# Kernel optimization log

Measured on AMD Instinct MI355X. Metric: run time of the kernel, lower is better.

The kernel has to match this reference:

```python
import jax, jax.numpy as jnp
import numpy as np

# Dims: batch, seq, model dim, heads, routes-per-query, bleed-over alpha
B, S, D, H, K_ROUTES = 4, 512, 1024, 16, 64
HD = D // H                      # head_dim = 64
SCALE = 1.0 / float(np.sqrt(HD))
ALPHA = 0.25                     # neighbor bleed-over (forward arg default 0.0; >0 here)
CAUSAL = True
NEG = jnp.float32(-1e9)


def _build_routes(seq_len: int, k: int, depth: int = 8) -> np.ndarray:
    """Cantor-coordinate based positional routes (mirrors _build_positional_routes)."""
    pos = np.arange(seq_len, dtype=np.float64)
    x = pos / max(1, seq_len - 1)
    x = np.clip(x, 1e-6, 1.0 - 1e-6)
    val = np.zeros_like(x)
    factor = 0.5
    for _ in range(depth):
        xs = x * 3.0
        digit = xs.astype(np.int64)
        frac = xs - digit
        val = val + (digit == 2).astype(np.float64) * factor
        x = frac
        factor *= 0.5
    coords = np.clip(val, 0.0, 1.0)
    dist = np.abs(coords[:, None] - coords[None, :])            # [S,S]
    routes = np.argsort(dist, axis=1, kind='stable')[:, :k]     # k smallest distances
    return routes.astype(np.int32)


def setup_inputs() -> dict:
    key = jax.random.key(0)
    k0, k1, k2 = jax.random.split(key, 3)
    x = jax.random.normal(k0, (B, S, D), dtype=jnp.float32)
    # nn.Linear weights stored pre-transposed as [in, out] for clean matmul
    w_qkv = jax.random.normal(k1, (D, 3 * D), dtype=jnp.float32) * (1.0 / np.sqrt(D))
    b_qkv = jnp.zeros((3 * D,), dtype=jnp.float32)
    w_out = jax.random.normal(k2, (D, D), dtype=jnp.float32) * (1.0 / np.sqrt(D))
    b_out = jnp.zeros((D,), dtype=jnp.float32)
    routes = jnp.asarray(_build_routes(S, K_ROUTES), dtype=jnp.int32)  # [S, K]
    return {"x": x, "w_qkv": w_qkv, "b_qkv": b_qkv,
            "w_out": w_out, "b_out": b_out, "routes": routes}


def reference(x, w_qkv, b_qkv, w_out, b_out, routes):
    # QKV projection: [B,S,3D] -> [3,B,H,S,hd]
    qkv = (x @ w_qkv + b_qkv).reshape(B, S, 3, H, HD).transpose(2, 0, 3, 1, 4)
    q, k, v = qkv[0], qkv[1], qkv[2]                 # each [B,H,S,hd]

    r = routes                                        # [S,K]
    k_g = jnp.take(k, r, axis=2)                      # [B,H,S,K,hd]
    v_g = jnp.take(v, r, axis=2)
    if ALPHA > 0.0:
        rl = jnp.clip(r - 1, 0, S - 1)
        rr = jnp.clip(r + 1, 0, S - 1)
        k_g = (1.0 - ALPHA) * k_g + (ALPHA / 2.0) * (jnp.take(k, rl, axis=2) + jnp.take(k, rr, axis=2))
        v_g = (1.0 - ALPHA) * v_g + (ALPHA / 2.0) * (jnp.take(v, rl, axis=2) + jnp.take(v, rr, axis=2))

    scores = jnp.einsum('bhqd,bhqkd->bhqk', q, k_g) * SCALE   # [B,H,S,K]
    if CAUSAL:
        # route index > query position is masked (each query always routes to itself)
        mask = r > jnp.arange(S, dtype=r.dtype)[:, None]       # [S,K]
        scores = jnp.where(mask[None, None], NEG, scores)

    attn = jax.nn.softmax(scores, axis=-1)
    out = jnp.einsum('bhqk,bhqkd->bhqd', attn, v_g)            # [B,H,S,hd]
    out = out.transpose(0, 2, 1, 3).reshape(B, S, D)
    return out @ w_out + b_out
```

## Files before the change

### kernel.cpp

```cpp
#include <hip/hip_runtime.h>
#include <hip/hip_bf16.h>

#define BB 4
#define SS 512
#define DD 1024
#define HH 16
#define KR 64
#define HDIM 64
#define THREE_D 3072
#define M_ROWS 2048
#define SCALE_F 0.125f
#define SCALE_LOG2E 0.1803368801111144f

typedef __attribute__((ext_vector_type(8))) short short8;
typedef __attribute__((ext_vector_type(4))) float floatx4;

union F8 { short8 s; unsigned int u[4]; unsigned short h[8]; };

__device__ inline float bfu(unsigned short h){ union{unsigned int u; float f;} c; c.u = ((unsigned int)h) << 16; return c.f; }
__device__ inline unsigned short f2bf(float f){
    union{float f; unsigned int u;} c; c.f = f;
    unsigned int u = c.u;
    return (unsigned short)((u + 0x7fffu + ((u >> 16) & 1u)) >> 16);
}

#define GLOAD_LDS16(g, l)                                                     \
    __builtin_amdgcn_global_load_lds(                                         \
        (const __attribute__((address_space(1))) unsigned int*)(g),           \
        (__attribute__((address_space(3))) unsigned int*)(l), 16, 0, 0)

__global__ __launch_bounds__(256) void prep_kernel(
    const float* __restrict__ x, const float* __restrict__ w_qkv,
    const float* __restrict__ w_out, const int* __restrict__ routes,
    unsigned short* __restrict__ xb_sw, unsigned short* __restrict__ wb1_sw,
    unsigned short* __restrict__ wb2_sw, unsigned int* __restrict__ maskg)
{
    const int bx = blockIdx.x;
    const int tid = threadIdx.x;
    if (bx < 1024) {
        int gid = bx * 256 + tid;
        int r  = gid & 127;
        int c  = (gid >> 7) & 3;
        int kt = (gid >> 9) & 31;
        int mt = gid >> 14;
        const float* src = x + ((size_t)(mt * 128 + r)) * 1024 + kt * 32 + c * 8;
        float4 a = *(const float4*)src;
        float4 b = *(const float4*)(src + 4);
        F8 o;
        o.h[0] = f2bf(a.x); o.h[1] = f2bf(a.y); o.h[2] = f2bf(a.z); o.h[3] = f2bf(a.w);
        o.h[4] = f2bf(b.x); o.h[5] = f2bf(b.y); o.h[6] = f2bf(b.z); o.h[7] = f2bf(b.w);
        *(uint4*)(xb_sw + (size_t)gid * 8) = *(uint4*)&o;
    } else if (bx < 3072) {
        const float* w;
        unsigned short* out;
        int gid, N;
        if (bx < 2560) { w = w_qkv; out = wb1_sw; N = THREE_D; gid = (bx - 1024) * 256 + tid; }
        else           { w = w_out; out = wb2_sw; N = DD;      gid = (bx - 2560) * 256 + tid; }
        int r  = gid & 127;
        int c  = (gid >> 7) & 3;
        int kt = (gid >> 9) & 31;
        int nt = gid >> 14;
        int n = nt * 128 + r;
        int kbase = kt * 32 + c * 8;
        F8 o;
#pragma unroll
        for (int j = 0; j < 8; ++j)
            o.h[j] = f2bf(w[(size_t)(kbase + j) * N + n]);
        *(uint4*)(out + (size_t)gid * 8) = *(uint4*)&o;
    } else {
        int q = (bx - 3072) * 256 + tid;
        unsigned int w[16];
#pragma unroll
        for (int i = 0; i < 16; ++i) w[i] = 0u;
        for (int j = 0; j < KR; ++j) {
            int r = routes[q * KR + j];
            if (r <= q) w[r >> 5] |= 1u << (r & 31);
        }
#pragma unroll
        for (int sw = 0; sw < 16; ++sw) maskg[sw * SS + q] = w[sw];
    }
}

__global__ __launch_bounds__(256) void gemm_qkv(
    const unsigned short* __restrict__ Asw,
    const unsigned short* __restrict__ Bsw,
    const float* __restrict__ bias,
    unsigned short* __restrict__ qb, unsigned short* __restrict__ kb,
    unsigned short* __restrict__ vb)
{
    __shared__ __align__(16) unsigned short Sh[24576];
    unsigned short* Alds = Sh;
    unsigned short* Blds = Sh + 8192;

    const int tid  = threadIdx.x;
    const int lane = tid & 63;
    const int wid  = tid >> 6;
    const int l15  = lane & 15;
    const int quad = lane >> 4;

    const int bid  = blockIdx.x;
    const int xcd  = bid & 7;
    const int loc  = bid >> 3;
    const int mt64 = (xcd & 3) * 8 + (loc & 7);
    const int nt   = (xcd >> 2) * 12 + (loc >> 3);

    const int mt = mt64 >> 1;
    const int rh = (mt64 & 1) * 64;
    const int wn = wid * 32;

    floatx4 acc[4][2];
#pragma unroll
    for (int i = 0; i < 4; ++i)
#pragma unroll
        for (int j = 0; j < 2; ++j) acc[i][j] = (floatx4){0.f, 0.f, 0.f, 0.f};

    for (int kt8 = 0; kt8 < 8; ++kt8) {
#pragma unroll
        for (int kh = 0; kh < 4; ++kh) {
            int kt = kt8 * 4 + kh;
            const unsigned short* ga = Asw + ((size_t)(mt * 32 + kt) * 4 + wid) * 1024 + (rh + lane) * 8;
            const unsigned short* gb = Bsw + (size_t)(nt * 32 + kt) * 4096 + wid * 1024 + lane * 8;
            GLOAD_LDS16(ga,       Alds + kh * 2048 + wid * 512 + lane * 8);
            GLOAD_LDS16(gb,       Blds + kh * 4096 + wid * 1024 + lane * 8);
            GLOAD_LDS16(gb + 512, Blds + kh * 4096 + wid * 1024 + 512 + lane * 8);
        }
        __syncthreads();

#pragma unroll
        for (int kh = 0; kh < 4; ++kh) {
            F8 af[4], bf[2];
#pragma unroll
            for (int mi = 0; mi < 4; ++mi)
                af[mi] = *(const F8*)(Alds + kh * 2048 + (size_t)(quad * 64 + mi * 16 + l15) * 8);
#pragma unroll
            for (int ni = 0; ni < 2; ++ni)
                bf[ni] = *(const F8*)(Blds + kh * 4096 + (size_t)(quad * 128 + wn + ni * 16 + l15) * 8);
#pragma unroll
            for (int mi = 0; mi < 4; ++mi)
#pragma unroll
                for (int ni = 0; ni < 2; ++ni)
                    acc[mi][ni] = __builtin_amdgcn_mfma_f32_16x16x32_bf16(
                        af[mi].s, bf[ni].s, acc[mi][ni], 0, 0, 0);
        }
        __syncthreads();
    }

    const int m0 = mt64 * 64;
    const int n0 = nt * 128;

#pragma unroll
    for (int mi = 0; mi < 4; ++mi) {
#pragma unroll
        for (int ni = 0; ni < 2; ++ni) {
            int col = wn + ni * 16 + l15;
            float bv = bias[n0 + col];
#pragma unroll
            for (int r = 0; r < 4; ++r) {
                int row = mi * 16 + quad * 4 + r;
                Sh[row * 136 + col] = f2bf(acc[mi][ni][r] + bv);
            }
        }
    }
    __syncthreads();

    for (int i = tid; i < 1024; i += 256) {
        int rr = i >> 4, cc = i & 15;
        int grow = m0 + rr, gcol = n0 + cc * 8;
        int b = grow >> 9, s = grow & 511;
        int which = gcol >> 10, rem = gcol & 1023;
        int h = rem >> 6, hd = rem & 63;
        unsigned short* dst = (which == 0) ? qb : (which == 1) ? kb : vb;
        uint4 val = *(const uint4*)(Sh + rr * 136 + cc * 8);
        *(uint4*)(dst + (((size_t)(b * HH + h) * SS) + s) * HDIM + hd) = val;
    }
}

__global__ __launch_bounds__(256) void gemm_out(
    const unsigned short* __restrict__ Asw,
    const unsigned short* __restrict__ Bsw,
    const float* __restrict__ bias,
    float* __restrict__ Cout)
{
    __shared__ __align__(16) unsigned short Alds[8192];
    __shared__ __align__(16) unsigned short Blds[8192];

    const int tid  = threadIdx.x;
    const int lane = tid & 63;
    const int wid  = tid >> 6;
    const int l15  = lane & 15;
    const int quad = lane >> 4;

    const int bid  = blockIdx.x;
    const int xcd  = bid & 7;
    const int loc  = bid >> 3;
    const int mt64 = (xcd & 3) * 8 + (loc & 7);
    const int nt64 = (xcd >> 2) * 8 + (loc >> 3);

    const int mt  = mt64 >> 1;
    const int rh  = (mt64 & 1) * 64;
    const int ntB = nt64 >> 1;
    const int rhB = (nt64 & 1) * 64;
    const int wm  = (wid >> 1) * 32;
    const int wn  = (wid & 1) * 32;

    floatx4 acc[2][2];
#pragma unroll
    for (int i = 0; i < 2; ++i)
#pragma unroll
        for (int j = 0; j < 2; ++j) acc[i][j] = (floatx4){0.f, 0.f, 0.f, 0.f};

    for (int kt4 = 0; kt4 < 8; ++kt4) {
#pragma unroll
        for (int kh = 0; kh < 4; ++kh) {
            int kt = kt4 * 4 + kh;
            const unsigned short* ga = Asw + ((size_t)(mt  * 32 + kt) * 4 + wid) * 1024 + (rh  + lane) * 8;
            const unsigned short* gb = Bsw + ((size_t)(ntB * 32 + kt) * 4 + wid) * 1024 + (rhB + lane) * 8;
            GLOAD_LDS16(ga, Alds + kh * 2048 + wid * 512 + lane * 8);
            GLOAD_LDS16(gb, Blds + kh * 2048 + wid * 512 + lane * 8);
        }
        __syncthreads();

#pragma unroll
        for (int kh = 0; kh < 4; ++kh) {
            F8 af[2], bf[2];
#pragma unroll
            for (int mi = 0; mi < 2; ++mi)
                af[mi] = *(const F8*)(Alds + kh * 2048 + (size_t)(quad * 64 + wm + mi * 16 + l15) * 8);
#pragma unroll
            for (int ni = 0; ni < 2; ++ni)
                bf[ni] = *(const F8*)(Blds + kh * 2048 + (size_t)(quad * 64 + wn + ni * 16 + l15) * 8);
#pragma unroll
            for (int mi = 0; mi < 2; ++mi)
#pragma unroll
                for (int ni = 0; ni < 2; ++ni)
                    acc[mi][ni] = __builtin_amdgcn_mfma_f32_16x16x32_bf16(
                        af[mi].s, bf[ni].s, acc[mi][ni], 0, 0, 0);
        }
        __syncthreads();
    }

    const int m0 = mt64 * 64;
    const int n0 = nt64 * 64;
#pragma unroll
    for (int mi = 0; mi < 2; ++mi) {
#pragma unroll
        for (int ni = 0; ni < 2; ++ni) {
            int col = n0 + wn + ni * 16 + l15;
            float bv = bias[col];
#pragma unroll
            for (int r = 0; r < 4; ++r) {
                int row = m0 + wm + mi * 16 + quad * 4 + r;
                Cout[(size_t)row * DD + col] = acc[mi][ni][r] + bv;
            }
        }
    }
}

__global__ __launch_bounds__(256) void blend_kv_kernel(
    const unsigned short* __restrict__ kb, const unsigned short* __restrict__ vb,
    unsigned short* __restrict__ K2g, unsigned short* __restrict__ Vtg)
{
    __shared__ float vt[130][65];
    const int bh = blockIdx.x >> 2;
    const int qd = blockIdx.x & 3;
    const int s0 = qd * 128;
    const int tid = threadIdx.x;
    const unsigned short* kbase = kb + (size_t)bh * SS * HDIM;
    const unsigned short* vbase = vb + (size_t)bh * SS * HDIM;
    unsigned short* Kq = K2g + ((size_t)(bh * 4 + qd)) * 8192;
    unsigned short* Vq = Vtg + ((size_t)(bh * 4 + qd)) * 8192;

    for (int i = tid; i < 130 * 8; i += 256) {
        int row = i >> 3, c8 = (i & 7) << 3;
        int s = s0 + row - 1; s = s < 0 ? 0 : (s > SS - 1 ? SS - 1 : s);
        F8 vv = *(const F8*)(vbase + (size_t)s * 64 + c8);
#pragma unroll
        for (int j = 0; j < 8; ++j) vt[row][c8 + j] = bfu(vv.h[j]);
    }

    for (int i = tid; i < 1024; i += 256) {
        int sl = i >> 3, cc = i & 7;
        int s = s0 + sl;
        int sm = s ? s - 1 : 0;
        int sp = (s < SS - 1) ? s + 1 : SS - 1;
        F8 k0 = *(const F8*)(kbase + (size_t)s  * 64 + cc * 8);
        F8 km = *(const F8*)(kbase + (size_t)sm * 64 + cc * 8);
        F8 kp = *(const F8*)(kbase + (size_t)sp * 64 + cc * 8);
        F8 o;
#pragma unroll
        for (int j = 0; j < 8; ++j)
            o.h[j] = f2bf(0.75f * bfu(k0.h[j]) + 0.125f * (bfu(km.h[j]) + bfu(kp.h[j])));
        *(uint4*)(Kq + (size_t)(sl * 8 + (cc ^ (sl & 7))) * 8) = *(uint4*)&o;
    }
    __syncthreads();

    for (int i = tid; i < 1024; i += 256) {
        int d = i >> 4, scl = i & 15;
        F8 o;
#pragma unroll
        for (int a = 0; a < 8; ++a) {
            int rl = scl * 8 + a;
            o.h[a] = f2bf(0.75f * vt[rl + 1][d] + 0.125f * (vt[rl][d] + vt[rl + 2][d]));
        }
        int chunk = d * 16 + (scl & 8) + ((scl ^ d) & 7);
        *(uint4*)(Vq + (size_t)chunk * 8) = *(uint4*)&o;
    }
}

__global__ __launch_bounds__(256) void attn_kernel(
    const unsigned short* __restrict__ qb,
    const unsigned short* __restrict__ K2g,
    const unsigned short* __restrict__ Vtg,
    const unsigned int* __restrict__ maskg,
    unsigned short* __restrict__ attn_sw)
{
    __shared__ __align__(16) unsigned short Ks2[2][8192];
    __shared__ __align__(16) unsigned short Vs2[2][8192];
    __shared__ __align__(16) unsigned short Ps[4096];

    const int bid = blockIdx.x;
    const int xcd = bid & 7;
    const int loc = bid >> 3;
    const int bh  = xcd * 8 + (loc & 7);
    const int qt8 = loc >> 3;
    const int qt  = (qt8 < 4) ? qt8 : 11 - qt8;
    const int b = bh >> 4, h = bh & 15;
    const int tid  = threadIdx.x;
    const int lane = tid & 63;
    const int wid  = tid >> 6;
    const int l15  = lane & 15;
    const int quad = lane >> 4;

    const int nq    = (qt >> 1) + 1;
    const int qmaxw = qt * 64 + wid * 16 + 15;

    const unsigned short* Kbh = K2g + (size_t)bh * 4 * 8192;
    const unsigned short* Vbh = Vtg + (size_t)bh * 4 * 8192;

    #define STAGE(qd, bufi) do {                                              \
        const unsigned short* kq = Kbh + (size_t)(qd) * 8192 + wid * 2048;    \
        const unsigned short* vq = Vbh + (size_t)(qd) * 8192 + wid * 2048;    \
        unsigned short* kl = Ks2[bufi] + wid * 2048;                          \
        unsigned short* vl = Vs2[bufi] + wid * 2048;                          \
        GLOAD_LDS16(kq + lane * 8,        kl + lane * 8);                     \
        GLOAD_LDS16(kq + 512 + lane * 8,  kl + 512 + lane * 8);               \
        GLOAD_LDS16(kq + 1024 + lane * 8, kl + 1024 + lane * 8);              \
        GLOAD_LDS16(kq + 1536 + lane * 8, kl + 1536 + lane * 8);              \
        GLOAD_LDS16(vq + lane * 8,        vl + lane * 8);                     \
        GLOAD_LDS16(vq + 512 + lane * 8,  vl + 512 + lane * 8);               \
        GLOAD_LDS16(vq + 1024 + lane * 8, vl + 1024 + lane * 8);              \
        GLOAD_LDS16(vq + 1536 + lane * 8, vl + 1536 + lane * 8);              \
    } while (0)

    const int q = qt * 64 + wid * 16 + l15;

    F8 qf[2];
    {
        const unsigned short* qrow = qb + ((size_t)bh * SS + q) * 64;
        qf[0] = *(const F8*)(qrow + quad * 8);
        qf[1] = *(const F8*)(qrow + 32 + quad * 8);
    }

    STAGE(0, 0);
    __syncthreads();

    floatx4 accO[4];
#pragma unroll
    for (int dt = 0; dt < 4; ++dt) accO[dt] = (floatx4){0.f, 0.f, 0.f, 0.f};
    float lsum = 0.f;
    unsigned int* Pw = (unsigned int*)Ps + wid * 512;

    for (int qd = 0; qd < nq; ++qd) {
        if (qd + 1 < nq) STAGE(qd + 1, (qd + 1) & 1);
        const unsigned short* Ksb = Ks2[qd & 1];
        const unsigned short* Vsb = Vs2[qd & 1];
        const int sbase128 = qd * 128;

        floatx4 accS[8];
#pragma unroll
        for (int st = 0; st < 8; ++st) {
            if (sbase128 + (st >> 2) * 64 <= qmaxw) {
                int srow = st * 16 + l15;
                const F8 k0 = *(const F8*)(Ksb + (((srow << 3) | ( quad      ^ (srow & 7))) << 3));
                const F8 k1 = *(const F8*)(Ksb + (((srow << 3) | ((4 + quad) ^ (srow & 7))) << 3));
                floatx4 a = (floatx4){0.f, 0.f, 0.f, 0.f};
                a = __builtin_amdgcn_mfma_f32_16x16x32_bf16(k0.s, qf[0].s, a, 0, 0, 0);
                a = __builtin_amdgcn_mfma_f32_16x16x32_bf16(k1.s, qf[1].s, a, 0, 0, 0);
                accS[st] = a;
            }
        }

#pragma unroll
        for (int ch2 = 0; ch2 < 2; ++ch2) {
            if (sbase128 + ch2 * 64 > qmaxw) continue;
            unsigned int mw0 = maskg[(qd * 4 + ch2 * 2) * SS + q];
            unsigned int mw1 = maskg[(qd * 4 + ch2 * 2 + 1) * SS + q];
#pragma unroll
            for (int t = 0; t < 4; ++t) {
                unsigned int mw = (t & 2) ? mw1 : mw0;
                int sbase = (t & 1) * 16 + quad * 4;
                floatx4 a = accS[ch2 * 4 + t];
                float e0 = ((mw >> (sbase + 0)) & 1u) ? exp2f(a[0] * SCALE_LOG2E) : 0.f;
                float e1 = ((mw >> (sbase + 1)) & 1u) ? exp2f(a[1] * SCALE_LOG2E) : 0.f;
                float e2 = ((mw >> (sbase + 2)) & 1u) ? exp2f(a[2] * SCALE_LOG2E) : 0.f;
                float e3 = ((mw >> (sbase + 3)) & 1u) ? exp2f(a[3] * SCALE_LOG2E) : 0.f;
                lsum += (e0 + e1) + (e2 + e3);
                unsigned int w0 = (unsigned int)f2bf(e0) | ((unsigned int)f2bf(e1) << 16);
                unsigned int w1 = (unsigned int)f2bf(e2) | ((unsigned int)f2bf(e3) << 16);
                int off0 = t * 8 + quad * 2;
                int off1 = off0 + 1;
                Pw[l15 * 32 + ((((off0 >> 2) ^ (l15 & 7)) << 2) | (off0 & 3))] = w0;
                Pw[l15 * 32 + ((((off1 >> 2) ^ (l15 & 7)) << 2) | (off1 & 3))] = w1;
            }
            F8 pa[2];
#pragma unroll
            for (int ks = 0; ks < 2; ++ks) {
                int ci = ks * 4 + quad;
                pa[ks] = *(const F8*)((const unsigned short*)(Pw + l15 * 32) +
                                      ((ci ^ (l15 & 7)) << 3));
            }
#pragma unroll
            for (int dt = 0; dt < 4; ++dt) {
                int d = dt * 16 + l15;
#pragma unroll
                for (int ks = 0; ks < 2; ++ks) {
                    int scl = ch2 * 8 + ks * 4 + quad;
                    int chunk = d * 16 + (scl & 8) + ((scl ^ d) & 7);
                    const F8 bv = *(const F8*)(Vsb + ((size_t)chunk << 3));
                    accO[dt] = __builtin_amdgcn_mfma_f32_16x16x32_bf16(pa[ks].s, bv.s, accO[dt], 0, 0, 0);
                }
            }
        }
        __syncthreads();
    }

    lsum += __shfl_xor(lsum, 16);
    lsum += __shfl_xor(lsum, 32);
    float inv = 1.0f / lsum;

    unsigned short* Ow = Ps + wid * 1024;
#pragma unroll
    for (int r = 0; r < 4; ++r) {
        float invr = __shfl(inv, quad * 4 + r);
#pragma unroll
        for (int dt = 0; dt < 4; ++dt)
            Ow[(quad * 4 + r) * 64 + dt * 16 + l15] = f2bf(accO[dt][r] * invr);
    }
#pragma unroll
    for (int i = 0; i < 2; ++i) {
        int ch = i * 64 + lane;
        int qlocal = ch >> 3, j = ch & 7;
        int qq = qt * 64 + wid * 16 + qlocal;
        int mrow = b * SS + qq;
        int mt = mrow >> 7, rr = mrow & 127;
        int kt2 = h * 2 + (j >> 2), c = j & 3;
        size_t gid = (((size_t)(mt * 32 + kt2) * 4 + c) * 128 + rr);
        *(uint4*)(attn_sw + gid * 8) = *(const uint4*)(Ow + qlocal * 64 + j * 8);
    }
    #undef STAGE
}

extern "C" void kernel_launch(void* const* d_in, const int* in_sizes, int n_in,
                              void* d_out, int out_size, void* d_ws, size_t ws_size,
                              hipStream_t stream)
{
    const float* x     = (const float*)d_in[0];
    const float* w_qkv = (const float*)d_in[1];
    const float* b_qkv = (const float*)d_in[2];
    const float* w_out = (const float*)d_in[3];
    const float* b_out = (const float*)d_in[4];
    const int* routes  = (const int*)d_in[5];

    char* w = (char*)d_ws;
    unsigned short* xb_sw  = (unsigned short*)(w);
    unsigned short* wb1_sw = (unsigned short*)(w + (4u  << 20));
    unsigned short* wb2_sw = (unsigned short*)(w + (10u << 20));
    unsigned short* qbuf   = (unsigned short*)(w + (12u << 20));
    unsigned short* kbuf   = (unsigned short*)(w + (16u << 20));
    unsigned short* vbuf   = (unsigned short*)(w + (20u << 20));
    unsigned short* K2g    = (unsigned short*)(w + (24u << 20));
    unsigned short* Vtg    = (unsigned short*)(w + (28u << 20));
    unsigned short* attnsw = (unsigned short*)(w + (32u << 20));
    unsigned int*   maskg  = (unsigned int*)(w + (36u << 20));

    prep_kernel<<<3074, 256, 0, stream>>>(x, w_qkv, w_out, routes,
                                          xb_sw, wb1_sw, wb2_sw, maskg);

    gemm_qkv<<<768, 256, 0, stream>>>(xb_sw, wb1_sw, b_qkv, qbuf, kbuf, vbuf);

    blend_kv_kernel<<<256, 256, 0, stream>>>(kbuf, vbuf, K2g, Vtg);

    attn_kernel<<<512, 256, 0, stream>>>(qbuf, K2g, Vtg, maskg, attnsw);

    gemm_out<<<512, 256, 0, stream>>>(attnsw, wb2_sw, b_out, (float*)d_out);
}
```

Measured before the change: 141.4 us.

## Fuse neighbor K/V blending into QKV GEMM epilogue, drop blend kernel

The QKV GEMM now computes an extra 16-row halo for K/V tiles so the neighbor bleed-over blend can be done in registers via lane shuffles in the epilogue. It writes the blended K and transposed V directly in the swizzled layouts the attention kernel expects. This removes the separate blend kernel launch and the round trip of raw K/V through global memory. In exchange, K/V blocks do about 25% more MFMA work and load extra A rows, and the epilogue is more complex, with boundary handling at sequence edges.

```diff
diff --git a/kernel.cpp b/kernel.cpp
--- a/kernel.cpp
+++ b/kernel.cpp
@@ -81,16 +81,16 @@
     }
 }
 
-__global__ __launch_bounds__(256) void gemm_qkv(
+__global__ __launch_bounds__(256, 3) void gemm_qkv_fused(
     const unsigned short* __restrict__ Asw,
     const unsigned short* __restrict__ Bsw,
     const float* __restrict__ bias,
-    unsigned short* __restrict__ qb, unsigned short* __restrict__ kb,
-    unsigned short* __restrict__ vb)
+    unsigned short* __restrict__ qb,
+    unsigned short* __restrict__ K2g,
+    unsigned short* __restrict__ Vtg)
 {
-    __shared__ __align__(16) unsigned short Sh[24576];
-    unsigned short* Alds = Sh;
-    unsigned short* Blds = Sh + 8192;
+    __shared__ __align__(16) unsigned short Sh[26624];
+    unsigned short* Blds = Sh + 10240;
 
     const int tid  = threadIdx.x;
     const int lane = tid & 63;
@@ -104,13 +104,21 @@
     const int mt64 = (xcd & 3) * 8 + (loc & 7);
     const int nt   = (xcd >> 2) * 12 + (loc >> 3);
 
-    const int mt = mt64 >> 1;
-    const int rh = (mt64 & 1) * 64;
-    const int wn = wid * 32;
-
-    floatx4 acc[4][2];
-#pragma unroll
-    for (int i = 0; i < 4; ++i)
+    const bool isQ = (nt < 8);
+    const int m0   = mt64 * 64;
+    const int n0   = nt * 128;
+    const int wn   = wid * 32;
+    const int base_m = isQ ? m0 : (m0 - 8);
+
+    int rA = base_m + lane;        rA = rA < 0 ? 0 : (rA > 2047 ? 2047 : rA);
+    int rB = base_m + 64 + l15;    rB = rB < 0 ? 0 : (rB > 2047 ? 2047 : rB);
+    const int cB = lane >> 4;
+    const size_t aOffA = ((size_t)(rA >> 7) * 128) * 1024 + (size_t)(rA & 127) * 8;
+    const size_t aOffB = ((size_t)(rB >> 7) * 128) * 1024 + (size_t)(rB & 127) * 8;
+
+    floatx4 acc[5][2];
+#pragma unroll
+    for (int i = 0; i < 5; ++i)
 #pragma unroll
         for (int j = 0; j < 2; ++j) acc[i][j] = (floatx4){0.f, 0.f, 0.f, 0.f};
 
@@ -118,9 +126,13 @@
 #pragma unroll
         for (int kh = 0; kh < 4; ++kh) {
             int kt = kt8 * 4 + kh;
-            const unsigned short* ga = Asw + ((size_t)(mt * 32 + kt) * 4 + wid) * 1024 + (rh + lane) * 8;
+            const unsigned short* ga = Asw + aOffA + (size_t)(kt * 4 + wid) * 1024;
+            GLOAD_LDS16(ga, Sh + kh * 2560 + wid * 512 + lane * 8);
+            if (!isQ && wid == 0) {
+                const unsigned short* ga2 = Asw + aOffB + (size_t)(kt * 4 + cB) * 1024;
+                GLOAD_LDS16(ga2, Sh + kh * 2560 + 2048 + lane * 8);
+            }
             const unsigned short* gb = Bsw + (size_t)(nt * 32 + kt) * 4096 + wid * 1024 + lane * 8;
-            GLOAD_LDS16(ga,       Alds + kh * 2048 + wid * 512 + lane * 8);
             GLOAD_LDS16(gb,       Blds + kh * 4096 + wid * 1024 + lane * 8);
             GLOAD_LDS16(gb + 512, Blds + kh * 4096 + wid * 1024 + 512 + lane * 8);
         }
@@ -128,50 +140,107 @@
 
 #pragma unroll
         for (int kh = 0; kh < 4; ++kh) {
-            F8 af[4], bf[2];
-#pragma unroll
-            for (int mi = 0; mi < 4; ++mi)
-                af[mi] = *(const F8*)(Alds + kh * 2048 + (size_t)(quad * 64 + mi * 16 + l15) * 8);
+            F8 af[5], bf[2];
+#pragma unroll
+            for (int emi = 0; emi < 4; ++emi)
+                af[emi] = *(const F8*)(Sh + kh * 2560 + (size_t)(quad * 64 + emi * 16 + l15) * 8);
+            if (!isQ)
+                af[4] = *(const F8*)(Sh + kh * 2560 + 2048 + (size_t)(quad * 16 + l15) * 8);
 #pragma unroll
             for (int ni = 0; ni < 2; ++ni)
                 bf[ni] = *(const F8*)(Blds + kh * 4096 + (size_t)(quad * 128 + wn + ni * 16 + l15) * 8);
 #pragma unroll
-            for (int mi = 0; mi < 4; ++mi)
+            for (int emi = 0; emi < 5; ++emi) {
+                if (emi == 4 && isQ) continue;
 #pragma unroll
                 for (int ni = 0; ni < 2; ++ni)
-                    acc[mi][ni] = __builtin_amdgcn_mfma_f32_16x16x32_bf16(
-                        af[mi].s, bf[ni].s, acc[mi][ni], 0, 0, 0);
-        }
-        __syncthreads();
-    }
-
-    const int m0 = mt64 * 64;
-    const int n0 = nt * 128;
-
-#pragma unroll
-    for (int mi = 0; mi < 4; ++mi) {
+                    acc[emi][ni] = __builtin_amdgcn_mfma_f32_16x16x32_bf16(
+                        af[emi].s, bf[ni].s, acc[emi][ni], 0, 0, 0);
+            }
+        }
+        __syncthreads();
+    }
+
+    if (isQ) {
+#pragma unroll
+        for (int mi = 0; mi < 4; ++mi) {
+#pragma unroll
+            for (int ni = 0; ni < 2; ++ni) {
+                int col = wn + ni * 16 + l15;
+                float bv = bias[n0 + col];
+#pragma unroll
+                for (int r = 0; r < 4; ++r) {
+                    int row = mi * 16 + quad * 4 + r;
+                    Sh[row * 136 + col] = f2bf(acc[mi][ni][r] + bv);
+                }
+            }
+        }
+        __syncthreads();
+        for (int i = tid; i < 1024; i += 256) {
+            int rr = i >> 4, cc = i & 15;
+            int grow = m0 + rr, gcol = n0 + cc * 8;
+            int b = grow >> 9, s = grow & 511;
+            int h = gcol >> 6, hd = gcol & 63;
+            uint4 val = *(const uint4*)(Sh + rr * 136 + cc * 8);
+            *(uint4*)(qb + (((size_t)(b * HH + h) * SS) + s) * HDIM + hd) = val;
+        }
+    } else {
+        const bool firstBlk = ((mt64 & 7) == 0);
+        const bool lastBlk  = ((mt64 & 7) == 7);
 #pragma unroll
         for (int ni = 0; ni < 2; ++ni) {
             int col = wn + ni * 16 + l15;
             float bv = bias[n0 + col];
 #pragma unroll
-            for (int r = 0; r < 4; ++r) {
-                int row = mi * 16 + quad * 4 + r;
-                Sh[row * 136 + col] = f2bf(acc[mi][ni][r] + bv);
-            }
-        }
-    }
-    __syncthreads();
-
-    for (int i = tid; i < 1024; i += 256) {
-        int rr = i >> 4, cc = i & 15;
-        int grow = m0 + rr, gcol = n0 + cc * 8;
-        int b = grow >> 9, s = grow & 511;
-        int which = gcol >> 10, rem = gcol & 1023;
-        int h = rem >> 6, hd = rem & 63;
-        unsigned short* dst = (which == 0) ? qb : (which == 1) ? kb : vb;
-        uint4 val = *(const uint4*)(Sh + rr * 136 + cc * 8);
-        *(uint4*)(dst + (((size_t)(b * HH + h) * SS) + s) * HDIM + hd) = val;
+            for (int emi = 0; emi < 5; ++emi) {
+                float c0 = acc[emi][ni][0];
+                float c3 = acc[emi][ni][3];
+                float lA = __shfl_up(c3, 16);
+                float lB = (emi > 0) ? __shfl(acc[emi - 1][ni][3], l15 + 48) : 0.f;
+                float left0 = (quad == 0) ? lB : lA;
+                float rA_ = __shfl_down(c0, 16);
+                float rB_ = (emi < 4) ? __shfl(acc[emi + 1][ni][0], l15) : 0.f;
+                float right3 = (quad == 3) ? rB_ : rA_;
+#pragma unroll
+                for (int r = 0; r < 4; ++r) {
+                    int t = emi * 16 + quad * 4 + r - 8;
+                    float c = acc[emi][ni][r];
+                    float lv = (r == 0) ? left0 : acc[emi][ni][r - 1];
+                    float rv = (r == 3) ? right3 : acc[emi][ni][r + 1];
+                    if (firstBlk && emi == 0 && quad == 2 && r == 0) lv = c;
+                    if (lastBlk  && emi == 4 && quad == 1 && r == 3) rv = c;
+                    float bl = 0.75f * c + 0.125f * (lv + rv) + bv;
+                    if (t >= 0 && t < 64) Sh[t * 136 + col] = f2bf(bl);
+                }
+            }
+        }
+        __syncthreads();
+
+        const int b   = m0 >> 9;
+        const int qd  = (m0 >> 7) & 3;
+        const int s0q = m0 & 127;
+        if (nt < 16) {
+            for (int i = tid; i < 1024; i += 256) {
+                int hl = i >> 9, t = (i >> 3) & 63, cc = i & 7;
+                int bh = b * 16 + (nt - 8) * 2 + hl;
+                int sl = s0q + t;
+                uint4 val = *(const uint4*)(Sh + t * 136 + hl * 64 + cc * 8);
+                *(uint4*)(K2g + ((size_t)(bh * 4 + qd)) * 8192 +
+                          (size_t)(sl * 8 + (cc ^ (sl & 7))) * 8) = val;
+            }
+        } else {
+            for (int i = tid; i < 1024; i += 256) {
+                int hl = i >> 9, d = (i >> 3) & 63, t8 = i & 7;
+                int bh = b * 16 + (nt - 16) * 2 + hl;
+                int scl = (s0q >> 3) + t8;
+                F8 o;
+#pragma unroll
+                for (int a = 0; a < 8; ++a)
+                    o.h[a] = Sh[(t8 * 8 + a) * 136 + hl * 64 + d];
+                int chunk = d * 16 + (scl & 8) + ((scl ^ d) & 7);
+                *(uint4*)(Vtg + ((size_t)(bh * 4 + qd)) * 8192 + (size_t)chunk * 8) = *(uint4*)&o;
+            }
+        }
     }
 }
 
@@ -253,57 +322,6 @@
                 Cout[(size_t)row * DD + col] = acc[mi][ni][r] + bv;
             }
         }
-    }
-}
-
-__global__ __launch_bounds__(256) void blend_kv_kernel(
-    const unsigned short* __restrict__ kb, const unsigned short* __restrict__ vb,
-    unsigned short* __restrict__ K2g, unsigned short* __restrict__ Vtg)
-{
-    __shared__ float vt[130][65];
-    const int bh = blockIdx.x >> 2;
-    const int qd = blockIdx.x & 3;
-    const int s0 = qd * 128;
-    const int tid = threadIdx.x;
-    const unsigned short* kbase = kb + (size_t)bh * SS * HDIM;
-    const unsigned short* vbase = vb + (size_t)bh * SS * HDIM;
-    unsigned short* Kq = K2g + ((size_t)(bh * 4 + qd)) * 8192;
-    unsigned short* Vq = Vtg + ((size_t)(bh * 4 + qd)) * 8192;
-
-    for (int i = tid; i < 130 * 8; i += 256) {
-        int row = i >> 3, c8 = (i & 7) << 3;
-        int s = s0 + row - 1; s = s < 0 ? 0 : (s > SS - 1 ? SS - 1 : s);
-        F8 vv = *(const F8*)(vbase + (size_t)s * 64 + c8);
-#pragma unroll
-        for (int j = 0; j < 8; ++j) vt[row][c8 + j] = bfu(vv.h[j]);
-    }
-
-    for (int i = tid; i < 1024; i += 256) {
-        int sl = i >> 3, cc = i & 7;
-        int s = s0 + sl;
-        int sm = s ? s - 1 : 0;
-        int sp = (s < SS - 1) ? s + 1 : SS - 1;
-        F8 k0 = *(const F8*)(kbase + (size_t)s  * 64 + cc * 8);
-        F8 km = *(const F8*)(kbase + (size_t)sm * 64 + cc * 8);
-        F8 kp = *(const F8*)(kbase + (size_t)sp * 64 + cc * 8);
-        F8 o;
-#pragma unroll
-        for (int j = 0; j < 8; ++j)
-            o.h[j] = f2bf(0.75f * bfu(k0.h[j]) + 0.125f * (bfu(km.h[j]) + bfu(kp.h[j])));
-        *(uint4*)(Kq + (size_t)(sl * 8 + (cc ^ (sl & 7))) * 8) = *(uint4*)&o;
-    }
-    __syncthreads();
-
-    for (int i = tid; i < 1024; i += 256) {
-        int d = i >> 4, scl = i & 15;
-        F8 o;
-#pragma unroll
-        for (int a = 0; a < 8; ++a) {
-            int rl = scl * 8 + a;
-            o.h[a] = f2bf(0.75f * vt[rl + 1][d] + 0.125f * (vt[rl][d] + vt[rl + 2][d]));
-        }
-        int chunk = d * 16 + (scl & 8) + ((scl ^ d) & 7);
-        *(uint4*)(Vq + (size_t)chunk * 8) = *(uint4*)&o;
     }
 }
 
@@ -476,8 +494,6 @@
     unsigned short* wb1_sw = (unsigned short*)(w + (4u  << 20));
     unsigned short* wb2_sw = (unsigned short*)(w + (10u << 20));
     unsigned short* qbuf   = (unsigned short*)(w + (12u << 20));
-    unsigned short* kbuf   = (unsigned short*)(w + (16u << 20));
-    unsigned short* vbuf   = (unsigned short*)(w + (20u << 20));
     unsigned short* K2g    = (unsigned short*)(w + (24u << 20));
     unsigned short* Vtg    = (unsigned short*)(w + (28u << 20));
     unsigned short* attnsw = (unsigned short*)(w + (32u << 20));
@@ -486,9 +502,8 @@
     prep_kernel<<<3074, 256, 0, stream>>>(x, w_qkv, w_out, routes,
                                           xb_sw, wb1_sw, wb2_sw, maskg);
 
-    gemm_qkv<<<768, 256, 0, stream>>>(xb_sw, wb1_sw, b_qkv, qbuf, kbuf, vbuf);
-
-    blend_kv_kernel<<<256, 256, 0, stream>>>(kbuf, vbuf, K2g, Vtg);
+    gemm_qkv_fused<<<768, 256, 0, stream>>>(xb_sw, wb1_sw, b_qkv,
+                                            qbuf, K2g, Vtg);
 
     attn_kernel<<<512, 256, 0, stream>>>(qbuf, K2g, Vtg, maskg, attnsw);
 
```

Result: faster. 138.4 us (-2.1%).
